# Kernel optimization log

Hardware: AMD Instinct MI355X
Metric: run time of the kernel (lower is better)

Reference implementation:

```python
import jax, jax.numpy as jnp
import numpy as np

# hyperparameters from init_kwargs
EPS = 1e-6
STEPSIZE = 0.5
BETA = 0.9
DELTA = 0.001

N, H, D, M = 1024, 8, 64, 64


def setup_inputs() -> dict:
    key0 = jax.random.key(0)
    ks = jax.random.split(key0, 9)
    return {
        "query": jax.random.normal(ks[0], (N, H, D), dtype=jnp.float32),
        "key": jax.random.normal(ks[1], (N, H, D), dtype=jnp.float32),
        "value": jax.random.normal(ks[2], (N, H, M), dtype=jnp.float32),
        "Siprev": jax.random.normal(ks[3], (N, H, D, M), dtype=jnp.float32),
        "Zi": jax.random.uniform(ks[4], (N, H, D), dtype=jnp.float32),
        "Pi": jax.random.normal(ks[5], (N, H, D, M), dtype=jnp.float32),
        "Mi": jax.random.uniform(ks[6], (N, H, D, M), dtype=jnp.float32),
        "Uiprev": jax.random.normal(ks[7], (N, H, D, M), dtype=jnp.float32),
        "Siprev2": jax.random.normal(ks[8], (N, H, D, M), dtype=jnp.float32),
    }


def _feature_map(x):
    # elu_feature_map: elu(x) + 1 (strictly positive features)
    return jax.nn.elu(x) + 1.0


def _fro_norm(x):
    # Frobenius norm over the (D, M) state dims, keepdims -> (N, H, 1, 1)
    return jnp.sqrt(jnp.sum(x * x, axis=(2, 3), keepdims=True))


def reference(query, key, value, Siprev, Zi, Pi, Mi, Uiprev, Siprev2):
    Q = _feature_map(query)            # (N, H, D)
    K = _feature_map(key)              # (N, H, D)

    Zi_new = Zi + K                    # (N, H, D)
    Ui = jnp.einsum('nhd,nhm->nhdm', K, value)  # (N, H, D, M)

    # Adamax-style momentum coefficient mu, per (n, h)
    mu = (1.0 - jnp.sqrt(STEPSIZE * _fro_norm(Ui - Uiprev) / _fro_norm(Siprev - Siprev2))) ** 2
    mu = jnp.clip(mu, 0.0, 1.0 - DELTA)

    Pi_new = mu * Pi - STEPSIZE * Ui
    Mi_new = jnp.maximum(BETA * Mi, jnp.abs(Ui))
    Si = Siprev - Pi_new / jnp.sqrt(Mi_new + 1e-16)

    Z = 1.0 / (jnp.einsum('nhd,nhd->nh', Q, Zi_new) + EPS)  # (N, H)
    V = jnp.einsum('nhd,nhdm,nh->nhm', Q, Si, Z)            # (N, H, M)
    return (V, Si, Zi_new, Pi_new, Mi_new, Ui, Siprev)
```

## Files before the change

### kernel.cpp

```cpp
#include <hip/hip_runtime.h>
#include <cstddef>


namespace {

constexpr float EPS      = 1e-6f;
constexpr float STEPSIZE = 0.5f;
constexpr float BETA     = 0.9f;
constexpr float DELTA    = 0.001f;

constexpr size_t NHD  = 1024ull * 8 * 64;
constexpr size_t NHDM = 1024ull * 8 * 64 * 64;

constexpr size_t OFF_V  = 0;
constexpr size_t OFF_SI = OFF_V  + NHD;
constexpr size_t OFF_ZN = OFF_SI + NHDM;
constexpr size_t OFF_PN = OFF_ZN + NHD;
constexpr size_t OFF_MN = OFF_PN + NHDM;
constexpr size_t OFF_UI = OFF_MN + NHDM;
constexpr size_t OFF_SP = OFF_UI + NHDM;

__device__ __forceinline__ float featmap(float x) {
    return x > 0.0f ? x + 1.0f : __expf(x);
}

}

__global__ __launch_bounds__(256)
void fra_adamax_fused(const float* __restrict__ query,
                      const float* __restrict__ key,
                      const float* __restrict__ value,
                      const float* __restrict__ Siprev,
                      const float* __restrict__ Zi,
                      const float* __restrict__ Pi,
                      const float* __restrict__ Mi,
                      const float* __restrict__ Uiprev,
                      const float* __restrict__ Siprev2,
                      float* __restrict__ out)
{
    __shared__ float  Qf[64];
    __shared__ float  Kf[64];
    __shared__ float4 Vl4[16];
    __shared__ float4 Sl[1024];
    __shared__ float  red[12];
    __shared__ float  bro[2];
    __shared__ float  vred[256];

    const int    t   = threadIdx.x;
    const int    nh  = blockIdx.x;
    const size_t vb  = (size_t)nh * 64;
    const size_t mb4 = (size_t)nh * 1024;

    float qz = 0.0f;
    if (t < 64) {
        float q  = featmap(query[vb + t]);
        float k  = featmap(key[vb + t]);
        float zn = Zi[vb + t] + k;
        Qf[t] = q;
        Kf[t] = k;
        out[OFF_ZN + vb + t] = zn;
        qz = q * zn;
    } else if (t < 128) {
        ((float*)Vl4)[t - 64] = value[vb + (t - 64)];
    }
    __syncthreads();

    const float4* Sp4  = (const float4*)Siprev  + mb4;
    const float4* Up4  = (const float4*)Uiprev  + mb4;
    const float4* Sp24 = (const float4*)Siprev2 + mb4;
    float4* oUi = (float4*)(out + OFF_UI) + mb4;
    float4* oSp = (float4*)(out + OFF_SP) + mb4;

    float4 ui[4], sp[4];
    float du = 0.0f, ds = 0.0f;
    #pragma unroll
    for (int j = 0; j < 4; ++j) {
        const int f4 = j * 256 + t;
        const int d  = f4 >> 4;
        const int mq = f4 & 15;
        const float  kd = Kf[d];
        const float4 v  = Vl4[mq];

        float4 u;
        u.x = kd * v.x; u.y = kd * v.y; u.z = kd * v.z; u.w = kd * v.w;

        const float4 up = Up4[f4];
        const float4 s  = Sp4[f4];
        const float4 s2 = Sp24[f4];

        float ex = u.x - up.x, ey = u.y - up.y, ez = u.z - up.z, ew = u.w - up.w;
        du += ex * ex + ey * ey + ez * ez + ew * ew;
        float fx = s.x - s2.x, fy = s.y - s2.y, fz = s.z - s2.z, fw = s.w - s2.w;
        ds += fx * fx + fy * fy + fz * fz + fw * fw;

        ui[j] = u;
        sp[j] = s;
        oUi[f4] = u;
        oSp[f4] = s;
    }

    #pragma unroll
    for (int off = 32; off > 0; off >>= 1) {
        du += __shfl_down(du, off);
        ds += __shfl_down(ds, off);
        qz += __shfl_down(qz, off);
    }
    const int wave = t >> 6;
    if ((t & 63) == 0) {
        red[wave]     = du;
        red[4 + wave] = ds;
        red[8 + wave] = qz;
    }
    __syncthreads();
    if (t == 0) {
        const float DU = red[0] + red[1] + red[2]  + red[3];
        const float DS = red[4] + red[5] + red[6]  + red[7];
        const float QZ = red[8] + red[9] + red[10] + red[11];
        const float n1 = sqrtf(DU);
        const float n2 = sqrtf(DS);
        const float r  = sqrtf(STEPSIZE * n1 / n2);
        const float om = 1.0f - r;
        float mu = om * om;
        mu = fminf(mu, 1.0f - DELTA);
        mu = fmaxf(mu, 0.0f);
        bro[0] = mu;
        bro[1] = 1.0f / (QZ + EPS);
    }
    __syncthreads();
    const float mu = bro[0];
    const float Z  = bro[1];

    const float4* Pi4 = (const float4*)Pi + mb4;
    const float4* Mi4 = (const float4*)Mi + mb4;
    float4* oSi = (float4*)(out + OFF_SI) + mb4;
    float4* oPn = (float4*)(out + OFF_PN) + mb4;
    float4* oMn = (float4*)(out + OFF_MN) + mb4;

    #pragma unroll
    for (int j = 0; j < 4; ++j) {
        const int f4 = j * 256 + t;
        const int d  = f4 >> 4;
        const float qd = Qf[d];
        const float4 p = Pi4[f4];
        const float4 m = Mi4[f4];
        const float4 u = ui[j];
        const float4 s = sp[j];

        float4 pn;
        pn.x = mu * p.x - STEPSIZE * u.x;
        pn.y = mu * p.y - STEPSIZE * u.y;
        pn.z = mu * p.z - STEPSIZE * u.z;
        pn.w = mu * p.w - STEPSIZE * u.w;

        float4 mn;
        mn.x = fmaxf(BETA * m.x, fabsf(u.x));
        mn.y = fmaxf(BETA * m.y, fabsf(u.y));
        mn.z = fmaxf(BETA * m.z, fabsf(u.z));
        mn.w = fmaxf(BETA * m.w, fabsf(u.w));

        float4 si;
        si.x = s.x - pn.x * rsqrtf(mn.x + 1e-16f);
        si.y = s.y - pn.y * rsqrtf(mn.y + 1e-16f);
        si.z = s.z - pn.z * rsqrtf(mn.z + 1e-16f);
        si.w = s.w - pn.w * rsqrtf(mn.w + 1e-16f);

        float4 qs;
        qs.x = qd * si.x; qs.y = qd * si.y; qs.z = qd * si.z; qs.w = qd * si.w;

        oPn[f4] = pn;
        oMn[f4] = mn;
        oSi[f4] = si;
        Sl[f4]  = qs;
    }
    __syncthreads();

    {
        const int m  = t & 63;
        const int d0 = (t >> 6) * 16;
        const float* S = (const float*)Sl;
        float acc = 0.0f;
        #pragma unroll
        for (int d = 0; d < 16; ++d)
            acc += S[(d0 + d) * 64 + m];
        vred[t] = acc;
    }
    __syncthreads();
    if (t < 64) {
        const float v = vred[t] + vred[t + 64] + vred[t + 128] + vred[t + 192];
        out[OFF_V + vb + t] = Z * v;
    }
}

extern "C" void kernel_launch(void* const* d_in, const int* in_sizes, int n_in,
                              void* d_out, int out_size, void* d_ws, size_t ws_size,
                              hipStream_t stream) {
    const float* query   = (const float*)d_in[0];
    const float* key     = (const float*)d_in[1];
    const float* value   = (const float*)d_in[2];
    const float* Siprev  = (const float*)d_in[3];
    const float* Zi      = (const float*)d_in[4];
    const float* Pi      = (const float*)d_in[5];
    const float* Mi      = (const float*)d_in[6];
    const float* Uiprev  = (const float*)d_in[7];
    const float* Siprev2 = (const float*)d_in[8];
    float* out = (float*)d_out;

    const int nh = in_sizes[0] / 64;
    fra_adamax_fused<<<nh, 256, 0, stream>>>(query, key, value, Siprev, Zi,
                                             Pi, Mi, Uiprev, Siprev2, out);
}
```

Measured before the change: 1.063 ms.

## Use nontemporal loads/stores, prefetch Pi/Mi early, and reduce V via shuffles

All streaming state loads and stores now use nontemporal builtins to avoid polluting cache. Pi and Mi are loaded before the mu reduction barrier so their latency overlaps the reduction. The Q·Si contraction is accumulated in registers and reduced with wave shuffles instead of staging a 16KB shared tile, which cuts LDS use and raises occupancy. Value is read directly per thread instead of through shared memory. This adds register pressure from holding four extra float4 arrays.

Result: faster. 1.034 ms (-2.7%).

```diff
diff --git a/kernel.cpp b/kernel.cpp
--- a/kernel.cpp
+++ b/kernel.cpp
@@ -19,6 +19,15 @@
 constexpr size_t OFF_MN = OFF_PN + NHDM;
 constexpr size_t OFF_UI = OFF_MN + NHDM;
 constexpr size_t OFF_SP = OFF_UI + NHDM;
+
+typedef float f4 __attribute__((ext_vector_type(4)));
+
+__device__ __forceinline__ f4 ntload(const f4* p) {
+    return __builtin_nontemporal_load(p);
+}
+__device__ __forceinline__ void ntstore(f4* p, f4 v) {
+    __builtin_nontemporal_store(v, p);
+}
 
 __device__ __forceinline__ float featmap(float x) {
     return x > 0.0f ? x + 1.0f : __expf(x);
@@ -38,65 +47,69 @@
                       const float* __restrict__ Siprev2,
                       float* __restrict__ out)
 {
-    __shared__ float  Qf[64];
-    __shared__ float  Kf[64];
-    __shared__ float4 Vl4[16];
-    __shared__ float4 Sl[1024];
-    __shared__ float  red[12];
-    __shared__ float  bro[2];
-    __shared__ float  vred[256];
+    __shared__ float Qf[64];
+    __shared__ float Kf[64];
+    __shared__ float red[12];
+    __shared__ float bro[2];
+    __shared__ f4    vpart[64];
 
     const int    t   = threadIdx.x;
     const int    nh  = blockIdx.x;
     const size_t vb  = (size_t)nh * 64;
     const size_t mb4 = (size_t)nh * 1024;
 
+    const f4 vrow = *((const f4*)value + (size_t)nh * 16 + (t & 15));
+
     float qz = 0.0f;
     if (t < 64) {
-        float q  = featmap(query[vb + t]);
-        float k  = featmap(key[vb + t]);
-        float zn = Zi[vb + t] + k;
+        const float q  = featmap(query[vb + t]);
+        const float k  = featmap(key[vb + t]);
+        const float zn = Zi[vb + t] + k;
         Qf[t] = q;
         Kf[t] = k;
         out[OFF_ZN + vb + t] = zn;
         qz = q * zn;
-    } else if (t < 128) {
-        ((float*)Vl4)[t - 64] = value[vb + (t - 64)];
-    }
-    __syncthreads();
-
-    const float4* Sp4  = (const float4*)Siprev  + mb4;
-    const float4* Up4  = (const float4*)Uiprev  + mb4;
-    const float4* Sp24 = (const float4*)Siprev2 + mb4;
-    float4* oUi = (float4*)(out + OFF_UI) + mb4;
-    float4* oSp = (float4*)(out + OFF_SP) + mb4;
-
-    float4 ui[4], sp[4];
+    }
+    __syncthreads();
+
+    const f4* Sp4  = (const f4*)Siprev  + mb4;
+    const f4* Up4  = (const f4*)Uiprev  + mb4;
+    const f4* Sp24 = (const f4*)Siprev2 + mb4;
+    const f4* Pi4  = (const f4*)Pi      + mb4;
+    const f4* Mi4  = (const f4*)Mi      + mb4;
+    f4* oUi = (f4*)(out + OFF_UI) + mb4;
+    f4* oSp = (f4*)(out + OFF_SP) + mb4;
+    f4* oSi = (f4*)(out + OFF_SI) + mb4;
+    f4* oPn = (f4*)(out + OFF_PN) + mb4;
+    f4* oMn = (f4*)(out + OFF_MN) + mb4;
+
+    f4 ui[4], sp[4], pr[4], mr[4];
     float du = 0.0f, ds = 0.0f;
     #pragma unroll
     for (int j = 0; j < 4; ++j) {
-        const int f4 = j * 256 + t;
-        const int d  = f4 >> 4;
-        const int mq = f4 & 15;
-        const float  kd = Kf[d];
-        const float4 v  = Vl4[mq];
-
-        float4 u;
-        u.x = kd * v.x; u.y = kd * v.y; u.z = kd * v.z; u.w = kd * v.w;
-
-        const float4 up = Up4[f4];
-        const float4 s  = Sp4[f4];
-        const float4 s2 = Sp24[f4];
-
-        float ex = u.x - up.x, ey = u.y - up.y, ez = u.z - up.z, ew = u.w - up.w;
-        du += ex * ex + ey * ey + ez * ez + ew * ew;
-        float fx = s.x - s2.x, fy = s.y - s2.y, fz = s.z - s2.z, fw = s.w - s2.w;
-        ds += fx * fx + fy * fy + fz * fz + fw * fw;
+        const int   f  = j * 256 + t;
+        const float kd = Kf[f >> 4];
+        const f4 up = ntload(Up4 + f);
+        const f4 s  = ntload(Sp4 + f);
+        const f4 s2 = ntload(Sp24 + f);
+
+        const f4 u = kd * vrow;
+        const f4 e = u - up;
+        du += e.x * e.x + e.y * e.y + e.z * e.z + e.w * e.w;
+        const f4 g = s - s2;
+        ds += g.x * g.x + g.y * g.y + g.z * g.z + g.w * g.w;
 
         ui[j] = u;
         sp[j] = s;
-        oUi[f4] = u;
-        oSp[f4] = s;
+        ntstore(oUi + f, u);
+        ntstore(oSp + f, s);
+    }
+
+    #pragma unroll
+    for (int j = 0; j < 4; ++j) {
+        const int f = j * 256 + t;
+        pr[j] = ntload(Pi4 + f);
+        mr[j] = ntload(Mi4 + f);
     }
 
     #pragma unroll
@@ -116,9 +129,7 @@
         const float DU = red[0] + red[1] + red[2]  + red[3];
         const float DS = red[4] + red[5] + red[6]  + red[7];
         const float QZ = red[8] + red[9] + red[10] + red[11];
-        const float n1 = sqrtf(DU);
-        const float n2 = sqrtf(DS);
-        const float r  = sqrtf(STEPSIZE * n1 / n2);
+        const float r  = sqrtf(STEPSIZE * sqrtf(DU) / sqrtf(DS));
         const float om = 1.0f - r;
         float mu = om * om;
         mu = fminf(mu, 1.0f - DELTA);
@@ -130,63 +141,49 @@
     const float mu = bro[0];
     const float Z  = bro[1];
 
-    const float4* Pi4 = (const float4*)Pi + mb4;
-    const float4* Mi4 = (const float4*)Mi + mb4;
-    float4* oSi = (float4*)(out + OFF_SI) + mb4;
-    float4* oPn = (float4*)(out + OFF_PN) + mb4;
-    float4* oMn = (float4*)(out + OFF_MN) + mb4;
-
+    f4 vacc = {0.0f, 0.0f, 0.0f, 0.0f};
     #pragma unroll
     for (int j = 0; j < 4; ++j) {
-        const int f4 = j * 256 + t;
-        const int d  = f4 >> 4;
-        const float qd = Qf[d];
-        const float4 p = Pi4[f4];
-        const float4 m = Mi4[f4];
-        const float4 u = ui[j];
-        const float4 s = sp[j];
-
-        float4 pn;
-        pn.x = mu * p.x - STEPSIZE * u.x;
-        pn.y = mu * p.y - STEPSIZE * u.y;
-        pn.z = mu * p.z - STEPSIZE * u.z;
-        pn.w = mu * p.w - STEPSIZE * u.w;
-
-        float4 mn;
+        const int   f  = j * 256 + t;
+        const float qd = Qf[f >> 4];
+        const f4 p = pr[j];
+        const f4 m = mr[j];
+        const f4 u = ui[j];
+        const f4 s = sp[j];
+
+        const f4 pn = mu * p - STEPSIZE * u;
+
+        f4 mn;
         mn.x = fmaxf(BETA * m.x, fabsf(u.x));
         mn.y = fmaxf(BETA * m.y, fabsf(u.y));
         mn.z = fmaxf(BETA * m.z, fabsf(u.z));
         mn.w = fmaxf(BETA * m.w, fabsf(u.w));
 
-        float4 si;
+        f4 si;
         si.x = s.x - pn.x * rsqrtf(mn.x + 1e-16f);
         si.y = s.y - pn.y * rsqrtf(mn.y + 1e-16f);
         si.z = s.z - pn.z * rsqrtf(mn.z + 1e-16f);
         si.w = s.w - pn.w * rsqrtf(mn.w + 1e-16f);
 
-        float4 qs;
-        qs.x = qd * si.x; qs.y = qd * si.y; qs.z = qd * si.z; qs.w = qd * si.w;
-
-        oPn[f4] = pn;
-        oMn[f4] = mn;
-        oSi[f4] = si;
-        Sl[f4]  = qs;
-    }
-    __syncthreads();
-
-    {
-        const int m  = t & 63;
-        const int d0 = (t >> 6) * 16;
-        const float* S = (const float*)Sl;
-        float acc = 0.0f;
-        #pragma unroll
-        for (int d = 0; d < 16; ++d)
-            acc += S[(d0 + d) * 64 + m];
-        vred[t] = acc;
-    }
+        ntstore(oPn + f, pn);
+        ntstore(oMn + f, mn);
+        ntstore(oSi + f, si);
+        vacc += qd * si;
+    }
+
+    #pragma unroll
+    for (int off = 32; off >= 16; off >>= 1) {
+        vacc.x += __shfl_down(vacc.x, off);
+        vacc.y += __shfl_down(vacc.y, off);
+        vacc.z += __shfl_down(vacc.z, off);
+        vacc.w += __shfl_down(vacc.w, off);
+    }
+    if ((t & 63) < 16)
+        vpart[wave * 16 + (t & 15)] = vacc;
     __syncthreads();
     if (t < 64) {
-        const float v = vred[t] + vred[t + 64] + vred[t + 128] + vred[t + 192];
+        const float* vp = (const float*)vpart;
+        const float v = vp[t] + vp[64 + t] + vp[128 + t] + vp[192 + t];
         out[OFF_V + vb + t] = Z * v;
     }
 }
```
